# Performance work log

Measured on AMD Instinct MI355X. Metric: run time of the kernel, lower is better.

## Reference

```python
import jax, jax.numpy as jnp
import numpy as np

N, E, D, H = 50000, 600000, 128, 128
SLOPE = 0.01  # default negative_slope of F.leaky_relu / nn.LeakyReLU


def leaky(x):
    return jnp.where(x >= 0, x, SLOPE * x)


def gcn_conv(x, src, dst, W, b, n):
    """PyG GCNConv: x' = D^{-1/2}(A+I)D^{-1/2} (x W) + b, symmetric norm with self-loops."""
    h = x @ W  # [n, out]
    ones = jnp.ones(src.shape[0], h.dtype)
    deg = jax.ops.segment_sum(ones, dst, num_segments=n) + 1.0  # +1 for self-loop
    dinv = jax.lax.rsqrt(deg)  # deg >= 1 always
    norm = dinv[src] * dinv[dst]  # per-edge coefficient
    msg = h[src] * norm[:, None]  # gather + scale: [E, out]
    agg = jax.ops.segment_sum(msg, dst, num_segments=n)  # scatter-add
    agg = agg + h * (dinv * dinv)[:, None]  # self-loop term
    return agg + b


def setup_inputs() -> dict:
    key = jax.random.key(0)
    ks = jax.random.split(key, 16)
    kaiming = lambda k, fi, fo: jax.random.normal(k, (fi, fo), jnp.float32) * np.sqrt(2.0 / fi)
    return {
        "x": jax.random.normal(ks[0], (N, D), jnp.float32),
        "edge_index": jax.random.randint(ks[1], (2, E), 0, N, jnp.int64 if jax.config.jax_enable_x64 else jnp.int32),
        "gen_data": jax.random.normal(ks[2], (N, H), jnp.float32),
        "Wc1": kaiming(ks[3], D, H), "bc1": jnp.zeros((H,), jnp.float32),
        "Wc2": kaiming(ks[4], H, H), "bc2": jnp.zeros((H,), jnp.float32),
        "Wm1": kaiming(ks[5], H, H), "bm1": jnp.zeros((H,), jnp.float32),
        "Wm2": kaiming(ks[6], H, H), "bm2": jnp.zeros((H,), jnp.float32),
        "Wp1": kaiming(ks[7], H, H), "bp1": jnp.zeros((H,), jnp.float32),
        "Wp2": kaiming(ks[8], H, H), "bp2": jnp.zeros((H,), jnp.float32),
    }


def reference(x, edge_index, gen_data, Wc1, bc1, Wc2, bc2, Wm1, bm1, Wm2, bm2, Wp1, bp1, Wp2, bp2):
    src, dst = edge_index[0], edge_index[1]
    lambd = 0.5
    # GraphEncoder4Link
    h = leaky(gcn_conv(x, src, dst, Wc1, bc1, N))
    h = leaky(gcn_conv(h, src, dst, Wc2, bc2, N) + h)
    h = leaky((leaky(h @ Wm1 + bm1) @ Wm2 + bm2) + h)
    # lambd interpolation with gen_data
    out = lambd * h + (1.0 - lambd) * gen_data
    # proj MLP
    out = leaky(leaky(out @ Wp1 + bp1) @ Wp2 + bp2)
    return out
```

## Files before the change

kernel.cpp:

```cpp
#include <hip/hip_runtime.h>
#include <cstdint>
#include <cstddef>

#define HH 128
#define SLOPE 0.01f

typedef __attribute__((ext_vector_type(8))) __bf16 bf16x8;
typedef __attribute__((ext_vector_type(8))) unsigned short ushort8v;
typedef __attribute__((ext_vector_type(4))) float f32x4;

__device__ __forceinline__ float lrelu(float x) { return x >= 0.f ? x : SLOPE * x; }
__device__ __forceinline__ unsigned short f2b(float f) {
  union { float f; unsigned u; } v; v.f = f;
  unsigned r = v.u + 0x7fffu + ((v.u >> 16) & 1u);
  return (unsigned short)(r >> 16);
}
__device__ __forceinline__ float b2f(unsigned short u) {
  union { unsigned u; float f; } v; v.u = ((unsigned)u) << 16; return v.f;
}

__device__ __forceinline__ int lofs(int r, int k) {
  return (r << 7) + ((((k >> 3) ^ r) & 15) << 3) + (k & 7);
}

#define WAVE_SYNC() asm volatile("s_waitcnt lgkmcnt(0)" ::: "memory")


__global__ __launch_bounds__(256) void count_kernel(const int* __restrict__ dst,
                                                    int* __restrict__ cnt, int nE) {
  int e = blockIdx.x * 256 + threadIdx.x;
  if (e < nE) atomicAdd(&cnt[dst[e]], 1);
}

__global__ __launch_bounds__(1024) void scan1_kernel(int* __restrict__ cnt,
                                                     int* __restrict__ rowptr,
                                                     int* __restrict__ bsum,
                                                     float* __restrict__ dinv, int n) {
  __shared__ int wsum[16];
  const int tid = threadIdx.x;
  const int lane = tid & 63, wid = tid >> 6;
  int i = blockIdx.x * 1024 + tid;
  int v = (i < n) ? cnt[i] : 0;
  int x = v;
#pragma unroll
  for (int off = 1; off < 64; off <<= 1) {
    int y = __shfl_up(x, off, 64);
    if (lane >= off) x += y;
  }
  if (lane == 63) wsum[wid] = x;
  __syncthreads();
  if (tid == 0) {
    int s = 0;
#pragma unroll
    for (int w = 0; w < 16; ++w) { int t = wsum[w]; wsum[w] = s; s += t; }
    bsum[blockIdx.x] = s;
  }
  __syncthreads();
  if (i < n) {
    rowptr[i] = wsum[wid] + x - v;
    dinv[i] = rsqrtf((float)v + 1.0f);
    cnt[i] = 0;
  }
}

__global__ __launch_bounds__(64) void scan2_kernel(int* __restrict__ bsum, int nb,
                                                   int* __restrict__ rowptr, int n, int E) {
  int lane = threadIdx.x;
  int v = (lane < nb) ? bsum[lane] : 0;
  int x = v;
#pragma unroll
  for (int off = 1; off < 64; off <<= 1) {
    int y = __shfl_up(x, off, 64);
    if (lane >= off) x += y;
  }
  if (lane < nb) bsum[lane] = x - v;
  if (lane == 0) rowptr[n] = E;
}

__global__ __launch_bounds__(1024) void scan3_kernel(int* __restrict__ rowptr,
                                                     const int* __restrict__ bsum, int n) {
  int i = blockIdx.x * 1024 + threadIdx.x;
  if (i < n) rowptr[i] += bsum[blockIdx.x];
}

__global__ __launch_bounds__(256) void fill_kernel(const int* __restrict__ src,
                                                   const int* __restrict__ dst,
                                                   const int* __restrict__ rowptr,
                                                   int* __restrict__ cursor,
                                                   const float* __restrict__ dinv,
                                                   int2* __restrict__ csr, int nE) {
  int e = blockIdx.x * 256 + threadIdx.x;
  if (e >= nE) return;
  int d = dst[e], s = src[e];
  int pos = rowptr[d] + atomicAdd(&cursor[d], 1);
  int2 ent;
  ent.x = s;
  ent.y = __float_as_int(dinv[s] * dinv[d]);
  csr[pos] = ent;
}

__global__ __launch_bounds__(256) void pack_kernel(const float* W0, const float* W1,
                                                   const float* W2, const float* W3,
                                                   const float* W4, const float* W5,
                                                   unsigned short* __restrict__ out) {
  const float* Ws[6] = {W0, W1, W2, W3, W4, W5};
  const float* W = Ws[blockIdx.y];
  int f = blockIdx.x * 256 + threadIdx.x;
  int j = f & 7, L = (f >> 3) & 63, c = (f >> 9) & 7, t = f >> 12;
  int k = t * 32 + (L >> 4) * 8 + j;
  int n = c * 16 + (L & 15);
  out[(size_t)blockIdx.y * 16384 + f] = f2b(W[k * HH + n]);
}


__device__ __forceinline__ void mfma_stage(const bf16x8 af[4], const bf16x8* __restrict__ Wf,
                                           int lane, f32x4 acc[8]) {
#pragma unroll
  for (int c = 0; c < 8; ++c) acc[c] = (f32x4){0.f, 0.f, 0.f, 0.f};
#pragma unroll
  for (int t = 0; t < 4; ++t) {
    bf16x8 wf[8];
#pragma unroll
    for (int c = 0; c < 8; ++c) wf[c] = Wf[(t * 8 + c) * 64 + lane];
#pragma unroll
    for (int c = 0; c < 8; ++c)
      acc[c] = __builtin_amdgcn_mfma_f32_16x16x32_bf16(af[t], wf[c], acc[c], 0, 0, 0);
  }
}

__device__ __forceinline__ void lds_afrags16(const unsigned short* __restrict__ Tl,
                                             int m, int quad, bf16x8 af[4]) {
#pragma unroll
  for (int t = 0; t < 4; ++t)
    af[t] = *(const bf16x8*)&Tl[lofs(m, t * 32 + quad * 8)];
}


__global__ __launch_bounds__(256, 1) void gemm_conv(const float* __restrict__ A,
                                                    const unsigned short* __restrict__ Wp,
                                                    unsigned short* __restrict__ out, int nrows) {
  const int tid = threadIdx.x;
  const int lane = tid & 63, wave = tid >> 6;
  const int row0 = blockIdx.x * 64 + wave * 16;
  const int m = lane & 15, quad = lane >> 4;
  const int gr = row0 + m;
  const bool rok = gr < nrows;
  const float* Arow = A + (size_t)gr * HH;

  bf16x8 af[4];
#pragma unroll
  for (int t = 0; t < 4; ++t) {
    const int k = t * 32 + quad * 8;
    float4 lo = make_float4(0.f, 0.f, 0.f, 0.f), hi = lo;
    if (rok) {
      lo = *(const float4*)(Arow + k);
      hi = *(const float4*)(Arow + k + 4);
    }
    union { ushort8v u; bf16x8 b; } cv;
    cv.u[0] = f2b(lo.x); cv.u[1] = f2b(lo.y); cv.u[2] = f2b(lo.z); cv.u[3] = f2b(lo.w);
    cv.u[4] = f2b(hi.x); cv.u[5] = f2b(hi.y); cv.u[6] = f2b(hi.z); cv.u[7] = f2b(hi.w);
    af[t] = cv.b;
  }

  f32x4 acc[8];
  mfma_stage(af, (const bf16x8*)Wp, lane, acc);

#pragma unroll
  for (int c = 0; c < 8; ++c) {
    int col = c * 16 + m;
#pragma unroll
    for (int g = 0; g < 4; ++g) {
      int row = row0 + quad * 4 + g;
      if (row < nrows) out[(size_t)row * HH + col] = f2b(acc[c][g]);
    }
  }
}


template <int RES, int OUTBF>
__global__ __launch_bounds__(256) void agg_kernel(const unsigned short* __restrict__ h,
                                                  const int* __restrict__ rowptr,
                                                  const int2* __restrict__ csr,
                                                  const float* __restrict__ dinv,
                                                  const float* __restrict__ bias,
                                                  const float* __restrict__ res,
                                                  void* __restrict__ outv, int n) {
  int node = blockIdx.x * 4 + (threadIdx.x >> 6);
  if (node >= n) return;
  int lane = threadIdx.x & 63;
  int c = lane << 1;
  int j = rowptr[node], end = rowptr[node + 1];
  float ax = 0.f, ay = 0.f;
  for (; j + 8 <= end; j += 8) {
    int2 e[8];
    ushort2 r[8];
#pragma unroll
    for (int q = 0; q < 8; ++q) e[q] = csr[j + q];
#pragma unroll
    for (int q = 0; q < 8; ++q) r[q] = *(const ushort2*)(h + (size_t)e[q].x * HH + c);
#pragma unroll
    for (int q = 0; q < 8; ++q) {
      float nv = __int_as_float(e[q].y);
      ax = fmaf(b2f(r[q].x), nv, ax); ay = fmaf(b2f(r[q].y), nv, ay);
    }
  }
  for (; j + 2 <= end; j += 2) {
    int2 e0 = csr[j], e1 = csr[j + 1];
    ushort2 r0 = *(const ushort2*)(h + (size_t)e0.x * HH + c);
    ushort2 r1 = *(const ushort2*)(h + (size_t)e1.x * HH + c);
    float n0 = __int_as_float(e0.y), n1 = __int_as_float(e1.y);
    ax = fmaf(b2f(r0.x), n0, ax); ay = fmaf(b2f(r0.y), n0, ay);
    ax = fmaf(b2f(r1.x), n1, ax); ay = fmaf(b2f(r1.y), n1, ay);
  }
  if (j < end) {
    int2 e0 = csr[j];
    float n0 = __int_as_float(e0.y);
    ushort2 r0 = *(const ushort2*)(h + (size_t)e0.x * HH + c);
    ax = fmaf(b2f(r0.x), n0, ax); ay = fmaf(b2f(r0.y), n0, ay);
  }
  float di = dinv[node], d2 = di * di;
  ushort2 hs = *(const ushort2*)(h + (size_t)node * HH + c);
  float2 b = *(const float2*)(bias + c);
  float ox = ax + b2f(hs.x) * d2 + b.x;
  float oy = ay + b2f(hs.y) * d2 + b.y;
  if (RES) {
    float2 r = *(const float2*)(res + (size_t)node * HH + c);
    ox += r.x; oy += r.y;
  }
  ox = lrelu(ox); oy = lrelu(oy);
  if (OUTBF) {
    ushort2 o; o.x = f2b(ox); o.y = f2b(oy);
    *(ushort2*)((unsigned short*)outv + (size_t)node * HH + c) = o;
  } else {
    *(float2*)((float*)outv + (size_t)node * HH + c) = make_float2(ox, oy);
  }
}


__global__ __launch_bounds__(256, 1) void fusedMLP(const unsigned short* __restrict__ f2bf,
                                                   const unsigned short* __restrict__ Wm1p,
                                                   const unsigned short* __restrict__ Wm2p,
                                                   const unsigned short* __restrict__ Wp1p,
                                                   const unsigned short* __restrict__ Wp2p,
                                                   const float* __restrict__ bm1,
                                                   const float* __restrict__ bm2,
                                                   const float* __restrict__ bp1,
                                                   const float* __restrict__ bp2,
                                                   const float* __restrict__ gen,
                                                   float* __restrict__ out, int n) {
  __shared__ __align__(16) unsigned short Ta[4][16 * HH];
  __shared__ __align__(16) unsigned short Tb[4][16 * HH];
  __shared__ __align__(16) float Bi[4][4 * HH];
  const int tid = threadIdx.x;
  const int lane = tid & 63, wave = tid >> 6;
  const int row0 = blockIdx.x * 64 + wave * 16;
  const int m = lane & 15, quad = lane >> 4;
  unsigned short* TA = Ta[wave];
  unsigned short* TB = Tb[wave];
  float* BI = Bi[wave];

#pragma unroll
  for (int i = 0; i < 4; ++i) {
    int idx = i * 64 + lane;
    int r = idx >> 4, k = (idx & 15) << 3;
    int gr = row0 + r;
    ushort8v v = {0, 0, 0, 0, 0, 0, 0, 0};
    if (gr < n) v = *(const ushort8v*)(f2bf + (size_t)gr * HH + k);
    *(ushort8v*)&TA[lofs(r, k)] = v;
  }

  ushort4 genb[8];
#pragma unroll
  for (int i = 0; i < 8; ++i) {
    int idx = i * 64 + lane;
    int r = idx >> 5, c4 = (idx & 31) << 2;
    int gr = row0 + r;
    float4 v = make_float4(0.f, 0.f, 0.f, 0.f);
    if (gr < n) v = *(const float4*)(gen + (size_t)gr * HH + c4);
    genb[i].x = f2b(v.x); genb[i].y = f2b(v.y); genb[i].z = f2b(v.z); genb[i].w = f2b(v.w);
  }

  {
    const float* b01 = (lane < 32) ? bm1 : bm2;
    const float* b23 = (lane < 32) ? bp1 : bp2;
    int col = (lane & 31) << 2;
    float4 v0 = *(const float4*)(b01 + col);
    float4 v1 = *(const float4*)(b23 + col);
    *(float4*)&BI[lane * 4] = v0;
    *(float4*)&BI[256 + lane * 4] = v1;
  }
  WAVE_SYNC();

  bf16x8 af[4];
  f32x4 acc[8];
  float bv[8];

#pragma unroll
  for (int cc = 0; cc < 8; ++cc) bv[cc] = BI[cc * 16 + m];
  lds_afrags16(TA, m, quad, af);
  mfma_stage(af, (const bf16x8*)Wm1p, lane, acc);
#pragma unroll
  for (int cc = 0; cc < 8; ++cc) {
    int col = cc * 16 + m;
#pragma unroll
    for (int g = 0; g < 4; ++g)
      TB[lofs(quad * 4 + g, col)] = f2b(lrelu(acc[cc][g] + bv[cc]));
  }
  WAVE_SYNC();

#pragma unroll
  for (int cc = 0; cc < 8; ++cc) bv[cc] = BI[128 + cc * 16 + m];
  lds_afrags16(TB, m, quad, af);
  WAVE_SYNC();
#pragma unroll
  for (int i = 0; i < 8; ++i) {
    int idx = i * 64 + lane;
    int r = idx >> 5, c4 = (idx & 31) << 2;
    *(ushort4*)&TB[lofs(r, c4)] = genb[i];
  }
  mfma_stage(af, (const bf16x8*)Wm2p, lane, acc);
  WAVE_SYNC();
#pragma unroll
  for (int cc = 0; cc < 8; ++cc) {
    int col = cc * 16 + m;
#pragma unroll
    for (int g = 0; g < 4; ++g) {
      int lr = quad * 4 + g;
      float f2v = b2f(TA[lofs(lr, col)]);
      float v = lrelu(acc[cc][g] + bv[cc] + f2v);
      float gv = b2f(TB[lofs(lr, col)]);
      TA[lofs(lr, col)] = f2b(0.5f * (v + gv));
    }
  }
  WAVE_SYNC();

#pragma unroll
  for (int cc = 0; cc < 8; ++cc) bv[cc] = BI[256 + cc * 16 + m];
  lds_afrags16(TA, m, quad, af);
  mfma_stage(af, (const bf16x8*)Wp1p, lane, acc);
#pragma unroll
  for (int cc = 0; cc < 8; ++cc) {
    int col = cc * 16 + m;
#pragma unroll
    for (int g = 0; g < 4; ++g)
      TB[lofs(quad * 4 + g, col)] = f2b(lrelu(acc[cc][g] + bv[cc]));
  }
  WAVE_SYNC();

#pragma unroll
  for (int cc = 0; cc < 8; ++cc) bv[cc] = BI[384 + cc * 16 + m];
  lds_afrags16(TB, m, quad, af);
  mfma_stage(af, (const bf16x8*)Wp2p, lane, acc);
#pragma unroll
  for (int cc = 0; cc < 8; ++cc) {
    int col = cc * 16 + m;
#pragma unroll
    for (int g = 0; g < 4; ++g) {
      int row = row0 + quad * 4 + g;
      if (row < n) out[(size_t)row * HH + col] = lrelu(acc[cc][g] + bv[cc]);
    }
  }
}


extern "C" void kernel_launch(void* const* d_in, const int* in_sizes, int n_in,
                              void* d_out, int out_size, void* d_ws, size_t ws_size,
                              hipStream_t stream) {
  const float* x   = (const float*)d_in[0];
  const int* ei    = (const int*)d_in[1];
  const float* gen = (const float*)d_in[2];
  const float* Wc1 = (const float*)d_in[3];
  const float* bc1 = (const float*)d_in[4];
  const float* Wc2 = (const float*)d_in[5];
  const float* bc2 = (const float*)d_in[6];
  const float* Wm1 = (const float*)d_in[7];
  const float* bm1 = (const float*)d_in[8];
  const float* Wm2 = (const float*)d_in[9];
  const float* bm2 = (const float*)d_in[10];
  const float* Wp1 = (const float*)d_in[11];
  const float* bp1 = (const float*)d_in[12];
  const float* Wp2 = (const float*)d_in[13];
  const float* bp2 = (const float*)d_in[14];

  const int N = in_sizes[0] / HH;
  const int E = in_sizes[1] / 2;
  const int* src = ei;
  const int* dst = ei + E;

  char* ws = (char*)d_ws;
  size_t off = 0;
  auto alloc = [&](size_t bytes) { void* p = ws + off; off += (bytes + 255) & ~(size_t)255; return p; };
  float* dinv            = (float*)alloc((size_t)N * 4);
  int*   rowptr          = (int*)  alloc((size_t)(N + 1) * 4);
  int*   cursor          = (int*)  alloc((size_t)N * 4);
  int*   bsum            = (int*)  alloc((size_t)64 * 4);
  int2*  csr             = (int2*) alloc((size_t)E * 8);
  unsigned short* h_bf   = (unsigned short*)alloc((size_t)N * HH * 2);
  unsigned short* t2_bf  = (unsigned short*)alloc((size_t)N * HH * 2);
  unsigned short* f2_bf  = (unsigned short*)alloc((size_t)N * HH * 2);
  float* f1_f32          = (float*)alloc((size_t)N * HH * 4);
  unsigned short* packed = (unsigned short*)alloc((size_t)6 * 16384 * 2);
  float* fOut = (float*)d_out;

  const int cblocks = (N + 63) / 64;
  const int eblocks = (E + 255) / 256;
  const int ablocks = (N + 3) / 4;
  const int sblocks = (N + 1023) / 1024;

  pack_kernel<<<dim3(64, 6), 256, 0, stream>>>(Wc1, Wc2, Wm1, Wm2, Wp1, Wp2, packed);

  hipMemsetAsync(cursor, 0, (size_t)N * 4, stream);
  count_kernel<<<eblocks, 256, 0, stream>>>(dst, cursor, E);
  scan1_kernel<<<sblocks, 1024, 0, stream>>>(cursor, rowptr, bsum, dinv, N);
  scan2_kernel<<<1, 64, 0, stream>>>(bsum, sblocks, rowptr, N, E);
  scan3_kernel<<<sblocks, 1024, 0, stream>>>(rowptr, bsum, N);
  fill_kernel<<<eblocks, 256, 0, stream>>>(src, dst, rowptr, cursor, dinv, csr, E);

  gemm_conv<<<cblocks, 256, 0, stream>>>(x, packed + 0 * 16384, h_bf, N);
  agg_kernel<0, 0><<<ablocks, 256, 0, stream>>>(h_bf, rowptr, csr, dinv, bc1, nullptr, f1_f32, N);
  gemm_conv<<<cblocks, 256, 0, stream>>>(f1_f32, packed + 1 * 16384, t2_bf, N);
  agg_kernel<1, 1><<<ablocks, 256, 0, stream>>>(t2_bf, rowptr, csr, dinv, bc2, f1_f32, f2_bf, N);
  fusedMLP<<<cblocks, 256, 0, stream>>>(f2_bf,
                                        packed + 2 * 16384, packed + 3 * 16384,
                                        packed + 4 * 16384, packed + 5 * 16384,
                                        bm1, bm2, bp1, bp2, gen, fOut, N);
}
```

Measured before the change: 300.3 us.

## Stage packed weight matrices in LDS for conv GEMM and fused MLP

Weight fragments were previously read by every wave directly from global memory. They are now loaded cooperatively once per block into a 32KB LDS buffer and read from there. In the fused MLP, the next layer's weights are prefetched into registers while the current layer computes, then swapped into LDS between block-wide barriers. This cuts redundant global/L2 weight traffic per block but adds __syncthreads barriers, higher LDS use that may lower occupancy, and drops the launch-bound minimum-blocks hint.

```diff
diff --git a/kernel.cpp b/kernel.cpp
--- a/kernel.cpp
+++ b/kernel.cpp
@@ -113,15 +113,16 @@
 }
 
 
-__device__ __forceinline__ void mfma_stage(const bf16x8 af[4], const bf16x8* __restrict__ Wf,
-                                           int lane, f32x4 acc[8]) {
+__device__ __forceinline__ void mfma_ldsW(const bf16x8 af[4],
+                                          const unsigned short* __restrict__ Wl,
+                                          int lane, f32x4 acc[8]) {
 #pragma unroll
   for (int c = 0; c < 8; ++c) acc[c] = (f32x4){0.f, 0.f, 0.f, 0.f};
 #pragma unroll
   for (int t = 0; t < 4; ++t) {
     bf16x8 wf[8];
 #pragma unroll
-    for (int c = 0; c < 8; ++c) wf[c] = Wf[(t * 8 + c) * 64 + lane];
+    for (int c = 0; c < 8; ++c) wf[c] = *(const bf16x8*)&Wl[(t * 8 + c) * 512 + lane * 8];
 #pragma unroll
     for (int c = 0; c < 8; ++c)
       acc[c] = __builtin_amdgcn_mfma_f32_16x16x32_bf16(af[t], wf[c], acc[c], 0, 0, 0);
@@ -136,17 +137,22 @@
 }
 
 
-__global__ __launch_bounds__(256, 1) void gemm_conv(const float* __restrict__ A,
-                                                    const unsigned short* __restrict__ Wp,
-                                                    unsigned short* __restrict__ out, int nrows) {
+__global__ __launch_bounds__(256) void gemm_conv(const float* __restrict__ A,
+                                                 const unsigned short* __restrict__ Wp,
+                                                 unsigned short* __restrict__ out, int nrows) {
+  __shared__ __align__(16) unsigned short Wl[16384];
   const int tid = threadIdx.x;
   const int lane = tid & 63, wave = tid >> 6;
   const int row0 = blockIdx.x * 64 + wave * 16;
   const int m = lane & 15, quad = lane >> 4;
+
+  uint4 pw[8];
+#pragma unroll
+  for (int i = 0; i < 8; ++i) pw[i] = ((const uint4*)Wp)[i * 256 + tid];
+
   const int gr = row0 + m;
   const bool rok = gr < nrows;
   const float* Arow = A + (size_t)gr * HH;
-
   bf16x8 af[4];
 #pragma unroll
   for (int t = 0; t < 4; ++t) {
@@ -162,8 +168,12 @@
     af[t] = cv.b;
   }
 
+#pragma unroll
+  for (int i = 0; i < 8; ++i) ((uint4*)Wl)[i * 256 + tid] = pw[i];
+  __syncthreads();
+
   f32x4 acc[8];
-  mfma_stage(af, (const bf16x8*)Wp, lane, acc);
+  mfma_ldsW(af, Wl, lane, acc);
 
 #pragma unroll
   for (int c = 0; c < 8; ++c) {
@@ -237,17 +247,18 @@
 }
 
 
-__global__ __launch_bounds__(256, 1) void fusedMLP(const unsigned short* __restrict__ f2bf,
-                                                   const unsigned short* __restrict__ Wm1p,
-                                                   const unsigned short* __restrict__ Wm2p,
-                                                   const unsigned short* __restrict__ Wp1p,
-                                                   const unsigned short* __restrict__ Wp2p,
-                                                   const float* __restrict__ bm1,
-                                                   const float* __restrict__ bm2,
-                                                   const float* __restrict__ bp1,
-                                                   const float* __restrict__ bp2,
-                                                   const float* __restrict__ gen,
-                                                   float* __restrict__ out, int n) {
+__global__ __launch_bounds__(256) void fusedMLP(const unsigned short* __restrict__ f2bf,
+                                                const unsigned short* __restrict__ Wm1p,
+                                                const unsigned short* __restrict__ Wm2p,
+                                                const unsigned short* __restrict__ Wp1p,
+                                                const unsigned short* __restrict__ Wp2p,
+                                                const float* __restrict__ bm1,
+                                                const float* __restrict__ bm2,
+                                                const float* __restrict__ bp1,
+                                                const float* __restrict__ bp2,
+                                                const float* __restrict__ gen,
+                                                float* __restrict__ out, int n) {
+  __shared__ __align__(16) unsigned short Wl[16384];
   __shared__ __align__(16) unsigned short Ta[4][16 * HH];
   __shared__ __align__(16) unsigned short Tb[4][16 * HH];
   __shared__ __align__(16) float Bi[4][4 * HH];
@@ -259,6 +270,10 @@
   unsigned short* TB = Tb[wave];
   float* BI = Bi[wave];
 
+  uint4 pw[8];
+#pragma unroll
+  for (int i = 0; i < 8; ++i) pw[i] = ((const uint4*)Wm1p)[i * 256 + tid];
+
 #pragma unroll
   for (int i = 0; i < 4; ++i) {
     int idx = i * 64 + lane;
@@ -289,7 +304,10 @@
     *(float4*)&BI[lane * 4] = v0;
     *(float4*)&BI[256 + lane * 4] = v1;
   }
-  WAVE_SYNC();
+
+#pragma unroll
+  for (int i = 0; i < 8; ++i) ((uint4*)Wl)[i * 256 + tid] = pw[i];
+  __syncthreads();
 
   bf16x8 af[4];
   f32x4 acc[8];
@@ -298,7 +316,9 @@
 #pragma unroll
   for (int cc = 0; cc < 8; ++cc) bv[cc] = BI[cc * 16 + m];
   lds_afrags16(TA, m, quad, af);
-  mfma_stage(af, (const bf16x8*)Wm1p, lane, acc);
+#pragma unroll
+  for (int i = 0; i < 8; ++i) pw[i] = ((const uint4*)Wm2p)[i * 256 + tid];
+  mfma_ldsW(af, Wl, lane, acc);
 #pragma unroll
   for (int cc = 0; cc < 8; ++cc) {
     int col = cc * 16 + m;
@@ -306,7 +326,12 @@
     for (int g = 0; g < 4; ++g)
       TB[lofs(quad * 4 + g, col)] = f2b(lrelu(acc[cc][g] + bv[cc]));
   }
-  WAVE_SYNC();
+  __syncthreads();
+#pragma unroll
+  for (int i = 0; i < 8; ++i) ((uint4*)Wl)[i * 256 + tid] = pw[i];
+#pragma unroll
+  for (int i = 0; i < 8; ++i) pw[i] = ((const uint4*)Wp1p)[i * 256 + tid];
+  __syncthreads();
 
 #pragma unroll
   for (int cc = 0; cc < 8; ++cc) bv[cc] = BI[128 + cc * 16 + m];
@@ -318,7 +343,7 @@
     int r = idx >> 5, c4 = (idx & 31) << 2;
     *(ushort4*)&TB[lofs(r, c4)] = genb[i];
   }
-  mfma_stage(af, (const bf16x8*)Wm2p, lane, acc);
+  mfma_ldsW(af, Wl, lane, acc);
   WAVE_SYNC();
 #pragma unroll
   for (int cc = 0; cc < 8; ++cc) {
@@ -332,12 +357,17 @@
       TA[lofs(lr, col)] = f2b(0.5f * (v + gv));
     }
   }
-  WAVE_SYNC();
+  __syncthreads();
+#pragma unroll
+  for (int i = 0; i < 8; ++i) ((uint4*)Wl)[i * 256 + tid] = pw[i];
+#pragma unroll
+  for (int i = 0; i < 8; ++i) pw[i] = ((const uint4*)Wp2p)[i * 256 + tid];
+  __syncthreads();
 
 #pragma unroll
   for (int cc = 0; cc < 8; ++cc) bv[cc] = BI[256 + cc * 16 + m];
   lds_afrags16(TA, m, quad, af);
-  mfma_stage(af, (const bf16x8*)Wp1p, lane, acc);
+  mfma_ldsW(af, Wl, lane, acc);
 #pragma unroll
   for (int cc = 0; cc < 8; ++cc) {
     int col = cc * 16 + m;
@@ -345,12 +375,15 @@
     for (int g = 0; g < 4; ++g)
       TB[lofs(quad * 4 + g, col)] = f2b(lrelu(acc[cc][g] + bv[cc]));
   }
-  WAVE_SYNC();
+  __syncthreads();
+#pragma unroll
+  for (int i = 0; i < 8; ++i) ((uint4*)Wl)[i * 256 + tid] = pw[i];
+  __syncthreads();
 
 #pragma unroll
   for (int cc = 0; cc < 8; ++cc) bv[cc] = BI[384 + cc * 16 + m];
   lds_afrags16(TB, m, quad, af);
-  mfma_stage(af, (const bf16x8*)Wp2p, lane, acc);
+  mfma_ldsW(af, Wl, lane, acc);
 #pragma unroll
   for (int cc = 0; cc < 8; ++cc) {
     int col = cc * 16 + m;
```

Result: slower. 314.8 us (+4.8%).
